# Optimization experiments

Measured on AMD Instinct MI355X. Metric: run time of the kernel, lower is better.

The kernel has to match this reference:

```python
import jax, jax.numpy as jnp
import numpy as np

D_MODEL = 1024
NHEADS = 16
D_K = D_MODEL // NHEADS


def setup_inputs() -> dict:
    key = jax.random.key(0)
    ks = jax.random.split(key, 12)
    B, S = 2, 2048
    scale = 1.0 / np.sqrt(D_MODEL)
    inp = {
        "query": jax.random.normal(ks[0], (B, S, D_MODEL), dtype=jnp.float32),
        "key": jax.random.normal(ks[1], (B, S, D_MODEL), dtype=jnp.float32),
        "value": jax.random.normal(ks[2], (B, S, D_MODEL), dtype=jnp.float32),
        "mask": jax.random.randint(ks[3], (B, 1, S, S), 0, 2, dtype=jnp.int32),
        "Wq": jax.random.normal(ks[4], (D_MODEL, D_MODEL), dtype=jnp.float32) * scale,
        "bq": jnp.zeros((D_MODEL,), dtype=jnp.float32),
        "Wk": jax.random.normal(ks[5], (D_MODEL, D_MODEL), dtype=jnp.float32) * scale,
        "bk": jnp.zeros((D_MODEL,), dtype=jnp.float32),
        "Wv": jax.random.normal(ks[6], (D_MODEL, D_MODEL), dtype=jnp.float32) * scale,
        "bv": jnp.zeros((D_MODEL,), dtype=jnp.float32),
        "Wo": jax.random.normal(ks[7], (D_MODEL, D_MODEL), dtype=jnp.float32) * scale,
        "bo": jnp.zeros((D_MODEL,), dtype=jnp.float32),
    }
    return inp


def _split_heads(x):
    # [B, S, (H*D)] -> [B, H, S, D]
    B, S, _ = x.shape
    return x.reshape(B, S, NHEADS, D_K).transpose(0, 2, 1, 3)


def reference(query, key, value, mask, Wq, bq, Wk, bk, Wv, bv, Wo, bo):
    B, Sq, _ = query.shape
    q = _split_heads(query @ Wq + bq)            # [B, H, Sq, Dk]
    k = _split_heads(key @ Wk + bk)              # [B, H, Sk, Dk]
    v = _split_heads(value @ Wv + bv)            # [B, H, Sk, Dk]
    # scores: [B, H, Sq, Sk], scaled by sqrt(d_k)
    scores = jnp.einsum("bhqd,bhkd->bhqk", q, k) / np.sqrt(D_K).astype(np.float32)
    scores = jnp.where(mask == 0, jnp.float32(-1e12), scores)
    weights = jax.nn.softmax(scores, axis=-1)
    out = jnp.einsum("bhqk,bhkd->bhqd", weights, v)  # [B, H, Sq, Dk]
    out = out.transpose(0, 2, 1, 3).reshape(B, Sq, D_MODEL)
    return out @ Wo + bo  # dropout is identity in eval / p=0
```

## Files before the change

### kernel.cpp

```cpp
#include <hip/hip_runtime.h>
#include <math.h>

#define D_MODEL 1024
#define NHEADS  16
#define DK      64
#define BATCH   2
#define SEQ     2048
#define M_TOTAL (BATCH * SEQ)
#define NT128   (SEQ / 128)
#define QSCALE 0.18033688011112042f

typedef __attribute__((ext_vector_type(8))) short bf16x8;
typedef __attribute__((ext_vector_type(4))) float f32x4;

__device__ __forceinline__ unsigned short f2bf(float f) {
    union { float f; unsigned int i; } v; v.f = f;
    return (unsigned short)((v.i + 0x7FFFu + ((v.i >> 16) & 1u)) >> 16);
}

__device__ __forceinline__ void async_copy16(const void* g, void* l) {
    __builtin_amdgcn_global_load_lds(
        (const __attribute__((address_space(1))) unsigned int*)g,
        (__attribute__((address_space(3))) unsigned int*)l, 16, 0, 0);
}

struct PrepArgs {
    const float* xs[3]; unsigned short* xd[3];
    const float* wsrc[4]; unsigned short* wdst[4];
    const int* mask; unsigned long long* wm;
};

__global__ __launch_bounds__(256)
void prep_all(const PrepArgs a)
{
    __shared__ unsigned short tbuf[32][33];
    const int id  = blockIdx.x;
    const int tid = threadIdx.x;

    if (id < 12288) {
        const int z = id >> 12;
        const int x = id & 4095;
        const float* __restrict__ s = a.xs[z];
        unsigned short* __restrict__ d = a.xd[z];
        const size_t i = ((size_t)x * 256 + tid) * 4;
        const float4 v = *reinterpret_cast<const float4*>(&s[i]);
        ushort4 o;
        o.x = f2bf(v.x); o.y = f2bf(v.y); o.z = f2bf(v.z); o.w = f2bf(v.w);
        *reinterpret_cast<ushort4*>(&d[i]) = o;
    } else if (id < 16384) {
        const int r  = id - 12288;
        const int z  = r >> 10;
        const int rem = r & 1023;
        const int bx = rem & 31;
        const int by = rem >> 5;
        const float* __restrict__ W = a.wsrc[z];
        unsigned short* __restrict__ WT = a.wdst[z];
        const int tx = tid & 31;
        const int ty = tid >> 5;
        const int nb = bx << 5;
        const int kb = by << 5;
#pragma unroll
        for (int i = 0; i < 4; ++i)
            tbuf[ty + (i << 3)][tx] =
                f2bf(W[(size_t)(kb + ty + (i << 3)) * D_MODEL + nb + tx]);
        __syncthreads();
#pragma unroll
        for (int i = 0; i < 4; ++i)
            WT[(size_t)(nb + ty + (i << 3)) * D_MODEL + kb + tx] =
                tbuf[tx][ty + (i << 3)];
    } else {
        const int bxm = id - 16384;
        const int lane = tid & 63;
        const int l15  = lane & 15;
        const int kg   = lane >> 4;
        const int wv   = (bxm << 2) + (tid >> 6);
        const int t    = wv & 31;
        const int qw   = (wv >> 5) & 127;
        const int bb   = wv >> 12;

        const int* mb = a.mask + (size_t)bb * SEQ * SEQ
                      + (size_t)((qw << 4) + l15) * SEQ + (t << 6) + (kg << 2);
        unsigned long long* wout = a.wm + ((((size_t)bb * 128 + qw) * 32 + t) << 4);

        int4 ln[4];
#pragma unroll
        for (int n = 0; n < 4; ++n)
            ln[n] = *reinterpret_cast<const int4*>(mb + (n << 4));
#pragma unroll
        for (int r = 0; r < 4; ++r)
#pragma unroll
            for (int n = 0; n < 4; ++n) {
                const int mvv = (&ln[n].x)[r];
                const unsigned long long bal = __ballot(mvv != 0);
                if (lane == 0) wout[(r << 2) | n] = bal;
            }
    }
}

template <typename OutT> struct GArgs {
    const unsigned short* X[3];
    const unsigned short* W[3];
    const float*          Bi[3];
    OutT*                 O[3];
    float                 scl[3];
};

__device__ __forceinline__ void st_out(float* p, float v) { *p = v; }
__device__ __forceinline__ void st_out(unsigned short* p, float v) { *p = f2bf(v); }

template <typename OutT, int MI>
__global__ __launch_bounds__(256)
void gemm_bf16(const GArgs<OutT> args, const int head_split)
{
    __shared__ __align__(16) unsigned short As[MI * 32][32];
    __shared__ __align__(16) unsigned short Bs[128][32];

    const int opz = blockIdx.z;
    const unsigned short* __restrict__ X  = args.X[opz];
    const unsigned short* __restrict__ WT = args.W[opz];
    const float* __restrict__ bias        = args.Bi[opz];
    OutT* __restrict__ out                = args.O[opz];
    const float scl                       = args.scl[opz];

    const int tid = threadIdx.x;
    const int wid = tid >> 6;
    const int wy  = wid >> 1;
    const int wx  = wid & 1;
    const int l15 = tid & 15;
    const int kg  = (tid >> 4) & 3;

    const int nwgy = (int)gridDim.y;
    const int id = ((int)blockIdx.y << 3) | (int)blockIdx.x;
    const int sw = (id & 7) * nwgy + (id >> 3);
    const int n0 = (sw & 7) << 7;
    const int m0 = (sw >> 3) * (MI * 32);

    const int lane = tid & 63;
    const int gr   = lane >> 2;
    const int gc   = (lane & 3) << 3;

    f32x4 acc[MI][4];
#pragma unroll
    for (int i = 0; i < MI; ++i)
#pragma unroll
        for (int j = 0; j < 4; ++j)
            acc[i][j] = (f32x4){0.f, 0.f, 0.f, 0.f};

#pragma unroll 1
    for (int t = 0; t < D_MODEL / 32; ++t) {
        const int k0 = t << 5;

        __syncthreads();
#pragma unroll
        for (int cc = 0; cc < 2; ++cc) {
            const int c = (wid << 1) + cc;
            async_copy16(&WT[(size_t)(n0 + (c << 4) + gr) * D_MODEL + k0 + gc],
                         &Bs[c << 4][0]);
            if (MI == 4)
                async_copy16(&X[(size_t)(m0 + (c << 4) + gr) * D_MODEL + k0 + gc],
                             &As[c << 4][0]);
        }
        if (MI == 2)
            async_copy16(&X[(size_t)(m0 + (wid << 4) + gr) * D_MODEL + k0 + gc],
                         &As[wid << 4][0]);
        __syncthreads();

        bf16x8 a[MI], b[4];
#pragma unroll
        for (int i = 0; i < MI; ++i)
            a[i] = *reinterpret_cast<const bf16x8*>(
                &As[(wy * MI + i) * 16 + l15][kg << 3]);
#pragma unroll
        for (int j = 0; j < 4; ++j)
            b[j] = *reinterpret_cast<const bf16x8*>(
                &Bs[(wx << 6) + (j << 4) + l15][kg << 3]);
#pragma unroll
        for (int i = 0; i < MI; ++i)
#pragma unroll
            for (int j = 0; j < 4; ++j)
                acc[i][j] = __builtin_amdgcn_mfma_f32_16x16x32_bf16(
                    a[i], b[j], acc[i][j], 0, 0, 0);
    }

    float bv[4];
#pragma unroll
    for (int j = 0; j < 4; ++j)
        bv[j] = bias[n0 + (wx << 6) + (j << 4) + l15];

#pragma unroll
    for (int i = 0; i < MI; ++i) {
#pragma unroll
        for (int r = 0; r < 4; ++r) {
            const int m = m0 + (wy * MI + i) * 16 + (kg << 2) + r;
#pragma unroll
            for (int j = 0; j < 4; ++j) {
                const int n = n0 + (wx << 6) + (j << 4) + l15;
                const float val = (acc[i][j][r] + bv[j]) * scl;
                if (head_split) {
                    const int bbx = m >> 11;
                    const int ss  = m & (SEQ - 1);
                    const int hhx = n >> 6;
                    const int dd  = n & (DK - 1);
                    st_out(&out[((size_t)(bbx * NHEADS + hhx) * SEQ + ss) * DK + dd], val);
                } else {
                    st_out(&out[(size_t)m * D_MODEL + n], val);
                }
            }
        }
    }
}

__global__ __launch_bounds__(256)
void flash_mfma(const unsigned short* __restrict__ Qb,
                const unsigned short* __restrict__ Kb,
                const unsigned short* __restrict__ Vb,
                const unsigned long long* __restrict__ wmask,
                unsigned short* __restrict__ ctx)
{
    __shared__ __align__(16) unsigned short Kbf[2][128][72];
    __shared__ __align__(16) unsigned short V3 [2][64][136];

    const int tid  = threadIdx.x;
    const int w    = tid >> 6;
    const int lane = tid & 63;
    const int l15  = lane & 15;
    const int kg   = lane >> 4;

    const int flat = ((int)blockIdx.z * NHEADS + (int)blockIdx.y) * (SEQ / 128)
                   + (int)blockIdx.x;
    const int swz  = ((flat & 7) << 6) | (flat >> 3);
    const int q0 = (swz & 15) << 7;
    const int hh = (swz >> 4) & 15;
    const int bb = swz >> 8;

    const unsigned short* Qh = Qb + (size_t)(bb * NHEADS + hh) * SEQ * DK;
    const unsigned short* Kh = Kb + (size_t)(bb * NHEADS + hh) * SEQ * DK;
    const unsigned short* Vh = Vb + (size_t)(bb * NHEADS + hh) * SEQ * DK;

    bf16x8 aq[2][2];
#pragma unroll
    for (int qi = 0; qi < 2; ++qi) {
        const unsigned short* qrow =
            Qh + (size_t)(q0 + w * 32 + qi * 16 + l15) * DK + (kg << 3);
        aq[qi][0] = *reinterpret_cast<const bf16x8*>(qrow);
        aq[qi][1] = *reinterpret_cast<const bf16x8*>(qrow + 32);
    }

    const int krow = tid >> 2;
    const int kcb  = (tid & 3) << 4;
    const int vkb  = (tid & 15) << 2;
    const int vdb  = (tid >> 4) << 2;
    const int q16  = tid & 15;
    const int voff = ((q16 & 3) << 5) | ((q16 >> 2) << 2);

    const int wbase0 = __builtin_amdgcn_readfirstlane(
        (bb * 128 + (q0 >> 4) + (w << 1)) << 9);
    const int wbase1 = wbase0 + 512;

    f32x4 lsum[2];
    f32x4 O4[2][4];
#pragma unroll
    for (int qi = 0; qi < 2; ++qi) {
        lsum[qi] = (f32x4){0.f, 0.f, 0.f, 0.f};
#pragma unroll
        for (int db = 0; db < 4; ++db) O4[qi][db] = (f32x4){0.f, 0.f, 0.f, 0.f};
    }

    uint4 kv0a = *reinterpret_cast<const uint4*>(Kh + (size_t)krow * DK + kcb);
    uint4 kv1a = *reinterpret_cast<const uint4*>(Kh + (size_t)krow * DK + kcb + 8);
    uint4 kv0b = *reinterpret_cast<const uint4*>(Kh + (size_t)(krow + 64) * DK + kcb);
    uint4 kv1b = *reinterpret_cast<const uint4*>(Kh + (size_t)(krow + 64) * DK + kcb + 8);
    uint2 vra[4], vrb[4];
#pragma unroll
    for (int i = 0; i < 4; ++i) {
        vra[i] = *reinterpret_cast<const uint2*>(Vh + (size_t)(vkb + i) * DK + vdb);
        vrb[i] = *reinterpret_cast<const uint2*>(Vh + (size_t)(64 + vkb + i) * DK + vdb);
    }

#pragma unroll 1
    for (int t = 0; t < NT128; ++t) {
        const int c = t & 1;

        *reinterpret_cast<uint4*>(&Kbf[c][krow][kcb])          = kv0a;
        *reinterpret_cast<uint4*>(&Kbf[c][krow][kcb + 8])      = kv1a;
        *reinterpret_cast<uint4*>(&Kbf[c][krow + 64][kcb])     = kv0b;
        *reinterpret_cast<uint4*>(&Kbf[c][krow + 64][kcb + 8]) = kv1b;
#pragma unroll
        for (int hf = 0; hf < 2; ++hf) {
            const uint2* vr = hf ? vrb : vra;
            const int vo = voff + (hf << 4);
            uint2 o;
            o.x = (vr[0].x & 0xFFFFu) | (vr[1].x << 16);
            o.y = (vr[2].x & 0xFFFFu) | (vr[3].x << 16);
            *reinterpret_cast<uint2*>(&V3[c][vdb + 0][vo]) = o;
            o.x = (vr[0].x >> 16) | (vr[1].x & 0xFFFF0000u);
            o.y = (vr[2].x >> 16) | (vr[3].x & 0xFFFF0000u);
            *reinterpret_cast<uint2*>(&V3[c][vdb + 1][vo]) = o;
            o.x = (vr[0].y & 0xFFFFu) | (vr[1].y << 16);
            o.y = (vr[2].y & 0xFFFFu) | (vr[3].y << 16);
            *reinterpret_cast<uint2*>(&V3[c][vdb + 2][vo]) = o;
            o.x = (vr[0].y >> 16) | (vr[1].y & 0xFFFF0000u);
            o.y = (vr[2].y >> 16) | (vr[3].y & 0xFFFF0000u);
            *reinterpret_cast<uint2*>(&V3[c][vdb + 3][vo]) = o;
        }
        __syncthreads();

        if (t + 1 < NT128) {
            const int kn = (t + 1) << 7;
            kv0a = *reinterpret_cast<const uint4*>(Kh + (size_t)(kn + krow) * DK + kcb);
            kv1a = *reinterpret_cast<const uint4*>(Kh + (size_t)(kn + krow) * DK + kcb + 8);
            kv0b = *reinterpret_cast<const uint4*>(Kh + (size_t)(kn + krow + 64) * DK + kcb);
            kv1b = *reinterpret_cast<const uint4*>(Kh + (size_t)(kn + krow + 64) * DK + kcb + 8);
#pragma unroll
            for (int i = 0; i < 4; ++i) {
                vra[i] = *reinterpret_cast<const uint2*>(
                    Vh + (size_t)(kn + vkb + i) * DK + vdb);
                vrb[i] = *reinterpret_cast<const uint2*>(
                    Vh + (size_t)(kn + 64 + vkb + i) * DK + vdb);
            }
        }

#pragma unroll
        for (int h = 0; h < 2; ++h) {
            f32x4 S[2][4];
#pragma unroll
            for (int n = 0; n < 4; ++n) {
                const bf16x8 b0 = *reinterpret_cast<const bf16x8*>(
                    &Kbf[c][(h << 6) + 16 * n + l15][kg << 3]);
                const bf16x8 b1 = *reinterpret_cast<const bf16x8*>(
                    &Kbf[c][(h << 6) + 16 * n + l15][(kg << 3) + 32]);
#pragma unroll
                for (int qi = 0; qi < 2; ++qi) {
                    f32x4 acc = (f32x4){0.f, 0.f, 0.f, 0.f};
                    acc = __builtin_amdgcn_mfma_f32_16x16x32_bf16(b0, aq[qi][0], acc, 0, 0, 0);
                    acc = __builtin_amdgcn_mfma_f32_16x16x32_bf16(b1, aq[qi][1], acc, 0, 0, 0);
                    S[qi][n] = acc;
                }
            }

            bf16x8 paf[2][2];
#pragma unroll
            for (int qi = 0; qi < 2; ++qi) {
                const unsigned long long* wmt =
                    wmask + (qi ? wbase1 : wbase0) + (((t << 1) | h) << 4);
                unsigned long long wmv[16];
#pragma unroll
                for (int rn = 0; rn < 16; ++rn) wmv[rn] = wmt[rn];

                unsigned pw01[4], pw23[4];
#pragma unroll
                for (int n = 0; n < 4; ++n) {
                    float xv[4];
#pragma unroll
                    for (int r = 0; r < 4; ++r) {
                        float e;
                        __asm__("v_exp_f32 %0, %1" : "=v"(e) : "v"(S[qi][n][r]));
                        __asm__("v_cndmask_b32 %0, 0, %1, %2"
                                : "=v"(e) : "v"(e), "s"(wmv[(r << 2) | n]));
                        xv[r] = e;
                    }
                    lsum[qi][0] += xv[0];
                    lsum[qi][1] += xv[1];
                    lsum[qi][2] += xv[2];
                    lsum[qi][3] += xv[3];
                    __asm__("v_cvt_pk_bf16_f32 %0, %1, %2"
                            : "=v"(pw01[n]) : "v"(xv[0]), "v"(xv[1]));
                    __asm__("v_cvt_pk_bf16_f32 %0, %1, %2"
                            : "=v"(pw23[n]) : "v"(xv[2]), "v"(xv[3]));
                }
                union { unsigned u[4]; bf16x8 v; } pa0, pa1;
                pa0.u[0] = pw01[0]; pa0.u[1] = pw23[0]; pa0.u[2] = pw01[1]; pa0.u[3] = pw23[1];
                pa1.u[0] = pw01[2]; pa1.u[1] = pw23[2]; pa1.u[2] = pw01[3]; pa1.u[3] = pw23[3];
                paf[qi][0] = pa0.v;
                paf[qi][1] = pa1.v;
            }

#pragma unroll
            for (int db = 0; db < 4; ++db) {
                const unsigned short* vbase =
                    &V3[c][(db << 4) + l15][(kg << 5) | (h << 4)];
                const bf16x8 v0 = *reinterpret_cast<const bf16x8*>(vbase);
                const bf16x8 v1 = *reinterpret_cast<const bf16x8*>(vbase + 8);
#pragma unroll
                for (int qi = 0; qi < 2; ++qi) {
                    O4[qi][db] = __builtin_amdgcn_mfma_f32_16x16x32_bf16(
                        paf[qi][0], v0, O4[qi][db], 0, 0, 0);
                    O4[qi][db] = __builtin_amdgcn_mfma_f32_16x16x32_bf16(
                        paf[qi][1], v1, O4[qi][db], 0, 0, 0);
                }
            }
        }
    }

#pragma unroll
    for (int qi = 0; qi < 2; ++qi) {
        float ls = (lsum[qi][0] + lsum[qi][1]) + (lsum[qi][2] + lsum[qi][3]);
        ls += __shfl_xor(ls, 16);
        ls += __shfl_xor(ls, 32);
#pragma unroll
        for (int r = 0; r < 4; ++r) {
            const float rs = __shfl(ls, (kg << 2) + r);
            const float inv = 1.f / rs;
            const size_t base =
                (size_t)(bb * SEQ + q0 + w * 32 + qi * 16 + (kg << 2) + r) * D_MODEL
                + hh * DK + l15;
#pragma unroll
            for (int db = 0; db < 4; ++db)
                ctx[base + 16 * db] = f2bf(O4[qi][db][r] * inv);
        }
    }
}

extern "C" void kernel_launch(void* const* d_in, const int* in_sizes, int n_in,
                              void* d_out, int out_size, void* d_ws, size_t ws_size,
                              hipStream_t stream)
{
    const float* query = (const float*)d_in[0];
    const float* key   = (const float*)d_in[1];
    const float* value = (const float*)d_in[2];
    const int*   mask  = (const int*)d_in[3];
    const float* Wq = (const float*)d_in[4];
    const float* bq = (const float*)d_in[5];
    const float* Wk = (const float*)d_in[6];
    const float* bk = (const float*)d_in[7];
    const float* Wv = (const float*)d_in[8];
    const float* bv = (const float*)d_in[9];
    const float* Wo = (const float*)d_in[10];
    const float* bo = (const float*)d_in[11];

    unsigned short* ws = (unsigned short*)d_ws;
    const size_t TE = (size_t)M_TOTAL * D_MODEL;
    const size_t WE = (size_t)D_MODEL * D_MODEL;
    unsigned short* Xq  = ws;
    unsigned short* Xk  = Xq + TE;
    unsigned short* Xv  = Xk + TE;
    unsigned short* WTq = Xv + TE;
    unsigned short* WTk = WTq + WE;
    unsigned short* WTv = WTk + WE;
    unsigned short* WTo = WTv + WE;
    unsigned short* Qb  = WTo + WE;
    unsigned short* Kb  = Qb + TE;
    unsigned short* Vb  = Kb + TE;
    unsigned short* Ctx = Vb + TE;
    unsigned long long* WM = (unsigned long long*)(Ctx + TE);

    PrepArgs pa;
    pa.xs[0] = query; pa.xs[1] = key; pa.xs[2] = value;
    pa.xd[0] = Xq;    pa.xd[1] = Xk;  pa.xd[2] = Xv;
    pa.wsrc[0] = Wq;  pa.wsrc[1] = Wk;  pa.wsrc[2] = Wv;  pa.wsrc[3] = Wo;
    pa.wdst[0] = WTq; pa.wdst[1] = WTk; pa.wdst[2] = WTv; pa.wdst[3] = WTo;
    pa.mask = mask; pa.wm = WM;
    prep_all<<<dim3(18432, 1, 1), 256, 0, stream>>>(pa);

    GArgs<unsigned short> qkv;
    qkv.X[0] = Xq;  qkv.X[1] = Xk;  qkv.X[2] = Xv;
    qkv.W[0] = WTq; qkv.W[1] = WTk; qkv.W[2] = WTv;
    qkv.Bi[0] = bq; qkv.Bi[1] = bk; qkv.Bi[2] = bv;
    qkv.O[0] = Qb;  qkv.O[1] = Kb;  qkv.O[2] = Vb;
    qkv.scl[0] = QSCALE; qkv.scl[1] = 1.f; qkv.scl[2] = 1.f;
    gemm_bf16<unsigned short, 4><<<dim3(8, 32, 3), 256, 0, stream>>>(qkv, 1);

    flash_mfma<<<dim3(SEQ / 128, NHEADS, BATCH), 256, 0, stream>>>(
        Qb, Kb, Vb, WM, Ctx);

    GArgs<float> op;
    op.X[0] = Ctx;  op.X[1] = Ctx;  op.X[2] = Ctx;
    op.W[0] = WTo;  op.W[1] = WTo;  op.W[2] = WTo;
    op.Bi[0] = bo;  op.Bi[1] = bo;  op.Bi[2] = bo;
    op.O[0] = (float*)d_out; op.O[1] = (float*)d_out; op.O[2] = (float*)d_out;
    op.scl[0] = 1.f; op.scl[1] = 1.f; op.scl[2] = 1.f;
    gemm_bf16<float, 2><<<dim3(8, 64, 1), 256, 0, stream>>>(op, 0);
}
```

Measured before the change: 258.7 us.

## Overlap Wo transpose and mask packing with QKV GEMM; row sums via MFMA

Moves the Wo transpose and the mask-to-bitmask packing out of the prep kernel into an extra z-plane of the QKV GEMM launch, so that work overlaps with the projection GEMM instead of running serially before it. Separately, the flash kernel now computes softmax row sums with an MFMA against a vector of ones instead of per-element VALU adds and cross-lane shuffles. The MFMA sum uses the bf16-rounded probabilities, which matches the values fed into PV but adds matrix-core work, and the extra plane's blocks are less regular in cost than the GEMM blocks.

```diff
diff --git a/kernel.cpp b/kernel.cpp
--- a/kernel.cpp
+++ b/kernel.cpp
@@ -26,8 +26,7 @@
 
 struct PrepArgs {
     const float* xs[3]; unsigned short* xd[3];
-    const float* wsrc[4]; unsigned short* wdst[4];
-    const int* mask; unsigned long long* wm;
+    const float* wsrc[3]; unsigned short* wdst[3];
 };
 
 __global__ __launch_bounds__(256)
@@ -47,7 +46,7 @@
         ushort4 o;
         o.x = f2bf(v.x); o.y = f2bf(v.y); o.z = f2bf(v.z); o.w = f2bf(v.w);
         *reinterpret_cast<ushort4*>(&d[i]) = o;
-    } else if (id < 16384) {
+    } else {
         const int r  = id - 12288;
         const int z  = r >> 10;
         const int rem = r & 1023;
@@ -68,32 +67,6 @@
         for (int i = 0; i < 4; ++i)
             WT[(size_t)(nb + ty + (i << 3)) * D_MODEL + kb + tx] =
                 tbuf[tx][ty + (i << 3)];
-    } else {
-        const int bxm = id - 16384;
-        const int lane = tid & 63;
-        const int l15  = lane & 15;
-        const int kg   = lane >> 4;
-        const int wv   = (bxm << 2) + (tid >> 6);
-        const int t    = wv & 31;
-        const int qw   = (wv >> 5) & 127;
-        const int bb   = wv >> 12;
-
-        const int* mb = a.mask + (size_t)bb * SEQ * SEQ
-                      + (size_t)((qw << 4) + l15) * SEQ + (t << 6) + (kg << 2);
-        unsigned long long* wout = a.wm + ((((size_t)bb * 128 + qw) * 32 + t) << 4);
-
-        int4 ln[4];
-#pragma unroll
-        for (int n = 0; n < 4; ++n)
-            ln[n] = *reinterpret_cast<const int4*>(mb + (n << 4));
-#pragma unroll
-        for (int r = 0; r < 4; ++r)
-#pragma unroll
-            for (int n = 0; n < 4; ++n) {
-                const int mvv = (&ln[n].x)[r];
-                const unsigned long long bal = __ballot(mvv != 0);
-                if (lane == 0) wout[(r << 2) | n] = bal;
-            }
     }
 }
 
@@ -105,15 +78,77 @@
     float                 scl[3];
 };
 
+struct PrepFuse {
+    const float* Wo;
+    unsigned short* WTo;
+    const int* mask;
+    unsigned long long* wm;
+};
+
 __device__ __forceinline__ void st_out(float* p, float v) { *p = v; }
 __device__ __forceinline__ void st_out(unsigned short* p, float v) { *p = f2bf(v); }
 
 template <typename OutT, int MI>
 __global__ __launch_bounds__(256)
-void gemm_bf16(const GArgs<OutT> args, const int head_split)
+void gemm_bf16(const GArgs<OutT> args, const PrepFuse fuse,
+               const int head_split, const int prep_plane)
 {
     __shared__ __align__(16) unsigned short As[MI * 32][32];
     __shared__ __align__(16) unsigned short Bs[128][32];
+
+    const int tid = threadIdx.x;
+
+    if (prep_plane >= 0 && (int)blockIdx.z == prep_plane) {
+        const int flat = ((int)blockIdx.y << 3) | (int)blockIdx.x;
+        unsigned short (*tb)[33] =
+            reinterpret_cast<unsigned short(*)[33]>(&As[0][0]);
+        const int tx = tid & 31;
+        const int ty = tid >> 5;
+#pragma unroll 1
+        for (int i = 0; i < 4; ++i) {
+            const int tt = (flat << 2) + i;
+            const int nb = (tt & 31) << 5;
+            const int kb = (tt >> 5) << 5;
+#pragma unroll
+            for (int j = 0; j < 4; ++j)
+                tb[ty + (j << 3)][tx] =
+                    f2bf(fuse.Wo[(size_t)(kb + ty + (j << 3)) * D_MODEL + nb + tx]);
+            __syncthreads();
+#pragma unroll
+            for (int j = 0; j < 4; ++j)
+                fuse.WTo[(size_t)(nb + ty + (j << 3)) * D_MODEL + kb + tx] =
+                    tb[tx][ty + (j << 3)];
+            __syncthreads();
+        }
+        const int wid_ = tid >> 6;
+        const int lane = tid & 63;
+        const int l15  = lane & 15;
+        const int kg   = lane >> 4;
+        const int ub   = (((flat << 2) + wid_) << 3);
+#pragma unroll 1
+        for (int i = 0; i < 8; ++i) {
+            const int u  = ub + i;
+            const int t  = u & 31;
+            const int qw = (u >> 5) & 127;
+            const int bb = u >> 12;
+            const int* mb = fuse.mask + (size_t)bb * SEQ * SEQ
+                          + (size_t)((qw << 4) + l15) * SEQ + (t << 6) + (kg << 2);
+            unsigned long long* wout =
+                fuse.wm + ((((size_t)bb * 128 + qw) * 32 + t) << 4);
+            int4 ln[4];
+#pragma unroll
+            for (int n = 0; n < 4; ++n)
+                ln[n] = *reinterpret_cast<const int4*>(mb + (n << 4));
+#pragma unroll
+            for (int r = 0; r < 4; ++r)
+#pragma unroll
+                for (int n = 0; n < 4; ++n) {
+                    const unsigned long long bal = __ballot((&ln[n].x)[r] != 0);
+                    if (lane == 0) wout[(r << 2) | n] = bal;
+                }
+        }
+        return;
+    }
 
     const int opz = blockIdx.z;
     const unsigned short* __restrict__ X  = args.X[opz];
@@ -122,7 +157,6 @@
     OutT* __restrict__ out                = args.O[opz];
     const float scl                       = args.scl[opz];
 
-    const int tid = threadIdx.x;
     const int wid = tid >> 6;
     const int wy  = wid >> 1;
     const int wx  = wid & 1;
@@ -257,11 +291,16 @@
         (bb * 128 + (q0 >> 4) + (w << 1)) << 9);
     const int wbase1 = wbase0 + 512;
 
-    f32x4 lsum[2];
+    union { unsigned u[4]; bf16x8 v; } onesu;
+#pragma unroll
+    for (int j = 0; j < 4; ++j) onesu.u[j] = 0x3F803F80u;
+    const bf16x8 onesv = onesu.v;
+
+    f32x4 Lacc[2];
     f32x4 O4[2][4];
 #pragma unroll
     for (int qi = 0; qi < 2; ++qi) {
-        lsum[qi] = (f32x4){0.f, 0.f, 0.f, 0.f};
+        Lacc[qi] = (f32x4){0.f, 0.f, 0.f, 0.f};
 #pragma unroll
         for (int db = 0; db < 4; ++db) O4[qi][db] = (f32x4){0.f, 0.f, 0.f, 0.f};
     }
@@ -359,10 +398,6 @@
                                 : "=v"(e) : "v"(e), "s"(wmv[(r << 2) | n]));
                         xv[r] = e;
                     }
-                    lsum[qi][0] += xv[0];
-                    lsum[qi][1] += xv[1];
-                    lsum[qi][2] += xv[2];
-                    lsum[qi][3] += xv[3];
                     __asm__("v_cvt_pk_bf16_f32 %0, %1, %2"
                             : "=v"(pw01[n]) : "v"(xv[0]), "v"(xv[1]));
                     __asm__("v_cvt_pk_bf16_f32 %0, %1, %2"
@@ -373,6 +408,11 @@
                 pa1.u[0] = pw01[2]; pa1.u[1] = pw23[2]; pa1.u[2] = pw01[3]; pa1.u[3] = pw23[3];
                 paf[qi][0] = pa0.v;
                 paf[qi][1] = pa1.v;
+
+                Lacc[qi] = __builtin_amdgcn_mfma_f32_16x16x32_bf16(
+                    paf[qi][0], onesv, Lacc[qi], 0, 0, 0);
+                Lacc[qi] = __builtin_amdgcn_mfma_f32_16x16x32_bf16(
+                    paf[qi][1], onesv, Lacc[qi], 0, 0, 0);
             }
 
 #pragma unroll
@@ -394,13 +434,9 @@
 
 #pragma unroll
     for (int qi = 0; qi < 2; ++qi) {
-        float ls = (lsum[qi][0] + lsum[qi][1]) + (lsum[qi][2] + lsum[qi][3]);
-        ls += __shfl_xor(ls, 16);
-        ls += __shfl_xor(ls, 32);
 #pragma unroll
         for (int r = 0; r < 4; ++r) {
-            const float rs = __shfl(ls, (kg << 2) + r);
-            const float inv = 1.f / rs;
+            const float inv = 1.f / Lacc[qi][r];
             const size_t base =
                 (size_t)(bb * SEQ + q0 + w * 32 + qi * 16 + (kg << 2) + r) * D_MODEL
                 + hh * DK + l15;
@@ -447,10 +483,12 @@
     PrepArgs pa;
     pa.xs[0] = query; pa.xs[1] = key; pa.xs[2] = value;
     pa.xd[0] = Xq;    pa.xd[1] = Xk;  pa.xd[2] = Xv;
-    pa.wsrc[0] = Wq;  pa.wsrc[1] = Wk;  pa.wsrc[2] = Wv;  pa.wsrc[3] = Wo;
-    pa.wdst[0] = WTq; pa.wdst[1] = WTk; pa.wdst[2] = WTv; pa.wdst[3] = WTo;
-    pa.mask = mask; pa.wm = WM;
-    prep_all<<<dim3(18432, 1, 1), 256, 0, stream>>>(pa);
+    pa.wsrc[0] = Wq;  pa.wsrc[1] = Wk;  pa.wsrc[2] = Wv;
+    pa.wdst[0] = WTq; pa.wdst[1] = WTk; pa.wdst[2] = WTv;
+    prep_all<<<dim3(15360, 1, 1), 256, 0, stream>>>(pa);
+
+    PrepFuse pf;
+    pf.Wo = Wo; pf.WTo = WTo; pf.mask = mask; pf.wm = WM;
 
     GArgs<unsigned short> qkv;
     qkv.X[0] = Xq;  qkv.X[1] = Xk;  qkv.X[2] = Xv;
@@ -458,7 +496,7 @@
     qkv.Bi[0] = bq; qkv.Bi[1] = bk; qkv.Bi[2] = bv;
     qkv.O[0] = Qb;  qkv.O[1] = Kb;  qkv.O[2] = Vb;
     qkv.scl[0] = QSCALE; qkv.scl[1] = 1.f; qkv.scl[2] = 1.f;
-    gemm_bf16<unsigned short, 4><<<dim3(8, 32, 3), 256, 0, stream>>>(qkv, 1);
+    gemm_bf16<unsigned short, 4><<<dim3(8, 32, 4), 256, 0, stream>>>(qkv, pf, 1, 3);
 
     flash_mfma<<<dim3(SEQ / 128, NHEADS, BATCH), 256, 0, stream>>>(
         Qb, Kb, Vb, WM, Ctx);
@@ -469,5 +507,6 @@
     op.Bi[0] = bo;  op.Bi[1] = bo;  op.Bi[2] = bo;
     op.O[0] = (float*)d_out; op.O[1] = (float*)d_out; op.O[2] = (float*)d_out;
     op.scl[0] = 1.f; op.scl[1] = 1.f; op.scl[2] = 1.f;
-    gemm_bf16<float, 2><<<dim3(8, 64, 1), 256, 0, stream>>>(op, 0);
+    PrepFuse pf0 = {};
+    gemm_bf16<float, 2><<<dim3(8, 64, 1), 256, 0, stream>>>(op, pf0, 0, -1);
 }
```

Measured after the change: 271.7 us. 5.0% more time.

## Fuse fp32-to-bf16 input conversion into QKV GEMM with double buffering; MFMA row sums

Applied to the files above, without the earlier changes.

Removes the separate fp32-to-bf16 conversion of query/key/value from the prep kernel. The QKV GEMM now loads fp32 activations into registers, converts them with packed bf16 instructions, and writes them to double-buffered LDS while prefetching the next K slice. This avoids writing and re-reading three bf16 copies of the inputs, at the cost of a more complex GEMM loop and more LDS. In the flash kernel, the softmax row sums are now computed with an extra MFMA against a ones vector, replacing scalar accumulation and shuffles. That row sum is taken from the bf16-rounded probabilities.

```diff
diff --git a/kernel.cpp b/kernel.cpp
--- a/kernel.cpp
+++ b/kernel.cpp
@@ -25,7 +25,6 @@
 }
 
 struct PrepArgs {
-    const float* xs[3]; unsigned short* xd[3];
     const float* wsrc[4]; unsigned short* wdst[4];
     const int* mask; unsigned long long* wm;
 };
@@ -37,20 +36,9 @@
     const int id  = blockIdx.x;
     const int tid = threadIdx.x;
 
-    if (id < 12288) {
-        const int z = id >> 12;
-        const int x = id & 4095;
-        const float* __restrict__ s = a.xs[z];
-        unsigned short* __restrict__ d = a.xd[z];
-        const size_t i = ((size_t)x * 256 + tid) * 4;
-        const float4 v = *reinterpret_cast<const float4*>(&s[i]);
-        ushort4 o;
-        o.x = f2bf(v.x); o.y = f2bf(v.y); o.z = f2bf(v.z); o.w = f2bf(v.w);
-        *reinterpret_cast<ushort4*>(&d[i]) = o;
-    } else if (id < 16384) {
-        const int r  = id - 12288;
-        const int z  = r >> 10;
-        const int rem = r & 1023;
+    if (id < 4096) {
+        const int z  = id >> 10;
+        const int rem = id & 1023;
         const int bx = rem & 31;
         const int by = rem >> 5;
         const float* __restrict__ W = a.wsrc[z];
@@ -69,7 +57,7 @@
             WT[(size_t)(nb + ty + (i << 3)) * D_MODEL + kb + tx] =
                 tbuf[tx][ty + (i << 3)];
     } else {
-        const int bxm = id - 16384;
+        const int bxm = id - 4096;
         const int lane = tid & 63;
         const int l15  = lane & 15;
         const int kg   = lane >> 4;
@@ -98,6 +86,7 @@
 }
 
 template <typename OutT> struct GArgs {
+    const float*          Xf[3];
     const unsigned short* X[3];
     const unsigned short* W[3];
     const float*          Bi[3];
@@ -108,15 +97,15 @@
 __device__ __forceinline__ void st_out(float* p, float v) { *p = v; }
 __device__ __forceinline__ void st_out(unsigned short* p, float v) { *p = f2bf(v); }
 
-template <typename OutT, int MI>
+template <typename OutT, int MI, bool AF32>
 __global__ __launch_bounds__(256)
 void gemm_bf16(const GArgs<OutT> args, const int head_split)
 {
-    __shared__ __align__(16) unsigned short As[MI * 32][32];
-    __shared__ __align__(16) unsigned short Bs[128][32];
+    constexpr int NB = AF32 ? 2 : 1;
+    __shared__ __align__(16) unsigned short As[NB][MI * 32][32];
+    __shared__ __align__(16) unsigned short Bs[NB][128][32];
 
     const int opz = blockIdx.z;
-    const unsigned short* __restrict__ X  = args.X[opz];
     const unsigned short* __restrict__ WT = args.W[opz];
     const float* __restrict__ bias        = args.Bi[opz];
     OutT* __restrict__ out                = args.O[opz];
@@ -146,40 +135,112 @@
         for (int j = 0; j < 4; ++j)
             acc[i][j] = (f32x4){0.f, 0.f, 0.f, 0.f};
 
+    if constexpr (AF32) {
+        const float* __restrict__ Xf = args.Xf[opz];
+        const int arow  = tid >> 1;
+        const int acol  = (tid & 1) << 4;
+
+        float4 ar[4];
+        {
+            const float* asrc = &Xf[(size_t)(m0 + arow) * D_MODEL + acol];
+#pragma unroll
+            for (int i = 0; i < 4; ++i)
+                ar[i] = *reinterpret_cast<const float4*>(asrc + (i << 2));
+        }
+#pragma unroll
+        for (int cc = 0; cc < 2; ++cc) {
+            const int cch = (wid << 1) + cc;
+            async_copy16(&WT[(size_t)(n0 + (cch << 4) + gr) * D_MODEL + gc],
+                         &Bs[0][cch << 4][0]);
+        }
+
 #pragma unroll 1
-    for (int t = 0; t < D_MODEL / 32; ++t) {
-        const int k0 = t << 5;
-
-        __syncthreads();
-#pragma unroll
-        for (int cc = 0; cc < 2; ++cc) {
-            const int c = (wid << 1) + cc;
-            async_copy16(&WT[(size_t)(n0 + (c << 4) + gr) * D_MODEL + k0 + gc],
-                         &Bs[c << 4][0]);
-            if (MI == 4)
-                async_copy16(&X[(size_t)(m0 + (c << 4) + gr) * D_MODEL + k0 + gc],
-                             &As[c << 4][0]);
-        }
-        if (MI == 2)
-            async_copy16(&X[(size_t)(m0 + (wid << 4) + gr) * D_MODEL + k0 + gc],
-                         &As[wid << 4][0]);
-        __syncthreads();
-
-        bf16x8 a[MI], b[4];
-#pragma unroll
-        for (int i = 0; i < MI; ++i)
-            a[i] = *reinterpret_cast<const bf16x8*>(
-                &As[(wy * MI + i) * 16 + l15][kg << 3]);
-#pragma unroll
-        for (int j = 0; j < 4; ++j)
-            b[j] = *reinterpret_cast<const bf16x8*>(
-                &Bs[(wx << 6) + (j << 4) + l15][kg << 3]);
-#pragma unroll
-        for (int i = 0; i < MI; ++i)
+        for (int t = 0; t < D_MODEL / 32; ++t) {
+            const int c = t & 1;
+
+            unsigned pw[8];
+#pragma unroll
+            for (int i = 0; i < 4; ++i) {
+                __asm__("v_cvt_pk_bf16_f32 %0, %1, %2"
+                        : "=v"(pw[2 * i]) : "v"(ar[i].x), "v"(ar[i].y));
+                __asm__("v_cvt_pk_bf16_f32 %0, %1, %2"
+                        : "=v"(pw[2 * i + 1]) : "v"(ar[i].z), "v"(ar[i].w));
+            }
+            union { unsigned u[4]; uint4 v; } q0, q1;
+            q0.u[0] = pw[0]; q0.u[1] = pw[1]; q0.u[2] = pw[2]; q0.u[3] = pw[3];
+            q1.u[0] = pw[4]; q1.u[1] = pw[5]; q1.u[2] = pw[6]; q1.u[3] = pw[7];
+            *reinterpret_cast<uint4*>(&As[c][arow][acol])     = q0.v;
+            *reinterpret_cast<uint4*>(&As[c][arow][acol + 8]) = q1.v;
+
+            __syncthreads();
+
+            if (t + 1 < D_MODEL / 32) {
+                const int k0n = (t + 1) << 5;
+                const float* asrc = &Xf[(size_t)(m0 + arow) * D_MODEL + k0n + acol];
+#pragma unroll
+                for (int i = 0; i < 4; ++i)
+                    ar[i] = *reinterpret_cast<const float4*>(asrc + (i << 2));
+#pragma unroll
+                for (int cc = 0; cc < 2; ++cc) {
+                    const int cch = (wid << 1) + cc;
+                    async_copy16(&WT[(size_t)(n0 + (cch << 4) + gr) * D_MODEL + k0n + gc],
+                                 &Bs[c ^ 1][cch << 4][0]);
+                }
+            }
+
+            bf16x8 a[MI], b[4];
+#pragma unroll
+            for (int i = 0; i < MI; ++i)
+                a[i] = *reinterpret_cast<const bf16x8*>(
+                    &As[c][(wy * MI + i) * 16 + l15][kg << 3]);
 #pragma unroll
             for (int j = 0; j < 4; ++j)
-                acc[i][j] = __builtin_amdgcn_mfma_f32_16x16x32_bf16(
-                    a[i], b[j], acc[i][j], 0, 0, 0);
+                b[j] = *reinterpret_cast<const bf16x8*>(
+                    &Bs[c][(wx << 6) + (j << 4) + l15][kg << 3]);
+#pragma unroll
+            for (int i = 0; i < MI; ++i)
+#pragma unroll
+                for (int j = 0; j < 4; ++j)
+                    acc[i][j] = __builtin_amdgcn_mfma_f32_16x16x32_bf16(
+                        a[i], b[j], acc[i][j], 0, 0, 0);
+        }
+    } else {
+        const unsigned short* __restrict__ X = args.X[opz];
+#pragma unroll 1
+        for (int t = 0; t < D_MODEL / 32; ++t) {
+            const int k0 = t << 5;
+
+            __syncthreads();
+#pragma unroll
+            for (int cc = 0; cc < 2; ++cc) {
+                const int c = (wid << 1) + cc;
+                async_copy16(&WT[(size_t)(n0 + (c << 4) + gr) * D_MODEL + k0 + gc],
+                             &Bs[0][c << 4][0]);
+                if (MI == 4)
+                    async_copy16(&X[(size_t)(m0 + (c << 4) + gr) * D_MODEL + k0 + gc],
+                                 &As[0][c << 4][0]);
+            }
+            if (MI == 2)
+                async_copy16(&X[(size_t)(m0 + (wid << 4) + gr) * D_MODEL + k0 + gc],
+                             &As[0][wid << 4][0]);
+            __syncthreads();
+
+            bf16x8 a[MI], b[4];
+#pragma unroll
+            for (int i = 0; i < MI; ++i)
+                a[i] = *reinterpret_cast<const bf16x8*>(
+                    &As[0][(wy * MI + i) * 16 + l15][kg << 3]);
+#pragma unroll
+            for (int j = 0; j < 4; ++j)
+                b[j] = *reinterpret_cast<const bf16x8*>(
+                    &Bs[0][(wx << 6) + (j << 4) + l15][kg << 3]);
+#pragma unroll
+            for (int i = 0; i < MI; ++i)
+#pragma unroll
+                for (int j = 0; j < 4; ++j)
+                    acc[i][j] = __builtin_amdgcn_mfma_f32_16x16x32_bf16(
+                        a[i], b[j], acc[i][j], 0, 0, 0);
+        }
     }
 
     float bv[4];
@@ -257,11 +318,16 @@
         (bb * 128 + (q0 >> 4) + (w << 1)) << 9);
     const int wbase1 = wbase0 + 512;
 
-    f32x4 lsum[2];
+    union { unsigned u[4]; bf16x8 v; } onesu;
+#pragma unroll
+    for (int j = 0; j < 4; ++j) onesu.u[j] = 0x3F803F80u;
+    const bf16x8 onesv = onesu.v;
+
+    f32x4 Lacc[2];
     f32x4 O4[2][4];
 #pragma unroll
     for (int qi = 0; qi < 2; ++qi) {
-        lsum[qi] = (f32x4){0.f, 0.f, 0.f, 0.f};
+        Lacc[qi] = (f32x4){0.f, 0.f, 0.f, 0.f};
 #pragma unroll
         for (int db = 0; db < 4; ++db) O4[qi][db] = (f32x4){0.f, 0.f, 0.f, 0.f};
     }
@@ -359,10 +425,6 @@
                                 : "=v"(e) : "v"(e), "s"(wmv[(r << 2) | n]));
                         xv[r] = e;
                     }
-                    lsum[qi][0] += xv[0];
-                    lsum[qi][1] += xv[1];
-                    lsum[qi][2] += xv[2];
-                    lsum[qi][3] += xv[3];
                     __asm__("v_cvt_pk_bf16_f32 %0, %1, %2"
                             : "=v"(pw01[n]) : "v"(xv[0]), "v"(xv[1]));
                     __asm__("v_cvt_pk_bf16_f32 %0, %1, %2"
@@ -373,6 +435,11 @@
                 pa1.u[0] = pw01[2]; pa1.u[1] = pw23[2]; pa1.u[2] = pw01[3]; pa1.u[3] = pw23[3];
                 paf[qi][0] = pa0.v;
                 paf[qi][1] = pa1.v;
+
+                Lacc[qi] = __builtin_amdgcn_mfma_f32_16x16x32_bf16(
+                    paf[qi][0], onesv, Lacc[qi], 0, 0, 0);
+                Lacc[qi] = __builtin_amdgcn_mfma_f32_16x16x32_bf16(
+                    paf[qi][1], onesv, Lacc[qi], 0, 0, 0);
             }
 
 #pragma unroll
@@ -394,13 +461,9 @@
 
 #pragma unroll
     for (int qi = 0; qi < 2; ++qi) {
-        float ls = (lsum[qi][0] + lsum[qi][1]) + (lsum[qi][2] + lsum[qi][3]);
-        ls += __shfl_xor(ls, 16);
-        ls += __shfl_xor(ls, 32);
 #pragma unroll
         for (int r = 0; r < 4; ++r) {
-            const float rs = __shfl(ls, (kg << 2) + r);
-            const float inv = 1.f / rs;
+            const float inv = 1.f / Lacc[qi][r];
             const size_t base =
                 (size_t)(bb * SEQ + q0 + w * 32 + qi * 16 + (kg << 2) + r) * D_MODEL
                 + hh * DK + l15;
@@ -431,10 +494,7 @@
     unsigned short* ws = (unsigned short*)d_ws;
     const size_t TE = (size_t)M_TOTAL * D_MODEL;
     const size_t WE = (size_t)D_MODEL * D_MODEL;
-    unsigned short* Xq  = ws;
-    unsigned short* Xk  = Xq + TE;
-    unsigned short* Xv  = Xk + TE;
-    unsigned short* WTq = Xv + TE;
+    unsigned short* WTq = ws;
     unsigned short* WTk = WTq + WE;
     unsigned short* WTv = WTk + WE;
     unsigned short* WTo = WTv + WE;
@@ -445,29 +505,29 @@
     unsigned long long* WM = (unsigned long long*)(Ctx + TE);
 
     PrepArgs pa;
-    pa.xs[0] = query; pa.xs[1] = key; pa.xs[2] = value;
-    pa.xd[0] = Xq;    pa.xd[1] = Xk;  pa.xd[2] = Xv;
     pa.wsrc[0] = Wq;  pa.wsrc[1] = Wk;  pa.wsrc[2] = Wv;  pa.wsrc[3] = Wo;
     pa.wdst[0] = WTq; pa.wdst[1] = WTk; pa.wdst[2] = WTv; pa.wdst[3] = WTo;
     pa.mask = mask; pa.wm = WM;
-    prep_all<<<dim3(18432, 1, 1), 256, 0, stream>>>(pa);
+    prep_all<<<dim3(6144, 1, 1), 256, 0, stream>>>(pa);
 
     GArgs<unsigned short> qkv;
-    qkv.X[0] = Xq;  qkv.X[1] = Xk;  qkv.X[2] = Xv;
+    qkv.Xf[0] = query; qkv.Xf[1] = key; qkv.Xf[2] = value;
+    qkv.X[0] = nullptr; qkv.X[1] = nullptr; qkv.X[2] = nullptr;
     qkv.W[0] = WTq; qkv.W[1] = WTk; qkv.W[2] = WTv;
     qkv.Bi[0] = bq; qkv.Bi[1] = bk; qkv.Bi[2] = bv;
     qkv.O[0] = Qb;  qkv.O[1] = Kb;  qkv.O[2] = Vb;
     qkv.scl[0] = QSCALE; qkv.scl[1] = 1.f; qkv.scl[2] = 1.f;
-    gemm_bf16<unsigned short, 4><<<dim3(8, 32, 3), 256, 0, stream>>>(qkv, 1);
+    gemm_bf16<unsigned short, 4, true><<<dim3(8, 32, 3), 256, 0, stream>>>(qkv, 1);
 
     flash_mfma<<<dim3(SEQ / 128, NHEADS, BATCH), 256, 0, stream>>>(
         Qb, Kb, Vb, WM, Ctx);
 
     GArgs<float> op;
+    op.Xf[0] = nullptr; op.Xf[1] = nullptr; op.Xf[2] = nullptr;
     op.X[0] = Ctx;  op.X[1] = Ctx;  op.X[2] = Ctx;
     op.W[0] = WTo;  op.W[1] = WTo;  op.W[2] = WTo;
     op.Bi[0] = bo;  op.Bi[1] = bo;  op.Bi[2] = bo;
     op.O[0] = (float*)d_out; op.O[1] = (float*)d_out; op.O[2] = (float*)d_out;
     op.scl[0] = 1.f; op.scl[1] = 1.f; op.scl[2] = 1.f;
-    gemm_bf16<float, 2><<<dim3(8, 64, 1), 256, 0, stream>>>(op, 0);
+    gemm_bf16<float, 2, false><<<dim3(8, 64, 1), 256, 0, stream>>>(op, 0);
 }
```

Measured after the change: 282.1 us. +9.0%, slower.
